# Performance work log

Measured on AMD Instinct MI355X. Metric: run time of the kernel, lower is better.

The kernel has to match this reference:

```python
import jax, jax.numpy as jnp
import numpy as np

D_MODEL = 2048
N_HEADS = 16
D_HEAD = 128
D_LATENT = 512


def setup_inputs() -> dict:
    key = jax.random.key(0)
    ks = jax.random.split(key, 5)
    s = lambda fan_in: 1.0 / np.sqrt(fan_in)
    x = jax.random.normal(ks[0], (2, 2048, D_MODEL), dtype=jnp.float32)
    # nn.Linear weights stored as [out, in]; we keep [in, out] for x @ W
    W_q = jax.random.uniform(ks[1], (D_MODEL, N_HEADS * D_HEAD), jnp.float32, -s(D_MODEL), s(D_MODEL))
    W_kv_down = jax.random.uniform(ks[2], (D_MODEL, D_LATENT), jnp.float32, -s(D_MODEL), s(D_MODEL))
    W_kv_up = jax.random.uniform(ks[3], (D_LATENT, N_HEADS * D_HEAD), jnp.float32, -s(D_LATENT), s(D_LATENT))
    W_o = jax.random.uniform(ks[4], (N_HEADS * D_HEAD, D_MODEL), jnp.float32, -s(N_HEADS * D_HEAD), s(N_HEADS * D_HEAD))
    return {"x": x, "W_q": W_q, "W_kv_down": W_kv_down, "W_kv_up": W_kv_up, "W_o": W_o}


def reference(x, W_q, W_kv_down, W_kv_up, W_o):
    B, S, _ = x.shape
    # q: [B, H, S, Dh]
    q = (x @ W_q).reshape(B, S, N_HEADS, D_HEAD).transpose(0, 2, 1, 3)
    # latent compression then up-projection; shared K = V
    latent = x @ W_kv_down                      # [B, S, Dl]
    kv = (latent @ W_kv_up).reshape(B, S, N_HEADS, D_HEAD).transpose(0, 2, 1, 3)
    scale = 1.0 / np.sqrt(D_HEAD).astype(np.float32)
    scores = jnp.einsum('bhqd,bhkd->bhqk', q, kv) * scale  # [B,H,S,S]
    probs = jax.nn.softmax(scores, axis=-1)
    out = jnp.einsum('bhqk,bhkd->bhqd', probs, kv)          # [B,H,S,Dh]
    out = out.transpose(0, 2, 1, 3).reshape(B, S, N_HEADS * D_HEAD)
    return out @ W_o
```

## Files before the change

### kernel.cpp

```cpp
#include <hip/hip_runtime.h>

typedef __attribute__((ext_vector_type(8))) __bf16 bf16x8;
typedef __attribute__((ext_vector_type(4))) float f32x4;
typedef __attribute__((ext_vector_type(16))) float f32x16;
typedef __attribute__((ext_vector_type(8))) unsigned short u16x8;
typedef __attribute__((ext_vector_type(4))) unsigned short u16x4;
typedef __attribute__((ext_vector_type(2))) unsigned int u32x2;
typedef __attribute__((ext_vector_type(4))) unsigned int u32x4;

#define MFMA16(a, b, c) __builtin_amdgcn_mfma_f32_16x16x32_bf16((a), (b), (c), 0, 0, 0)
#define MFMA32(a, b, c) __builtin_amdgcn_mfma_f32_32x32x16_bf16((a), (b), (c), 0, 0, 0)

__device__ __forceinline__ unsigned short f2bf(float f) {
    unsigned int u = __float_as_uint(f);
    unsigned int r = (u + 0x7FFFu + ((u >> 16) & 1u)) >> 16;
    return (unsigned short)r;
}

__device__ __forceinline__ float fexp2(float x) {
#if __has_builtin(__builtin_amdgcn_exp2f)
    return __builtin_amdgcn_exp2f(x);
#else
    return exp2f(x);
#endif
}

__device__ __forceinline__ u32x2 plswap32(unsigned int x, unsigned int y) {
#if __has_builtin(__builtin_amdgcn_permlane32_swap)
    return __builtin_amdgcn_permlane32_swap(x, y, false, false);
#else
    asm volatile("s_nop 1\n\tv_permlane32_swap_b32 %0, %1" : "+v"(x), "+v"(y));
    u32x2 r = {x, y};
    return r;
#endif
}
__device__ __forceinline__ u32x2 plswap16(unsigned int x, unsigned int y) {
#if __has_builtin(__builtin_amdgcn_permlane16_swap)
    return __builtin_amdgcn_permlane16_swap(x, y, false, false);
#else
    asm volatile("s_nop 1\n\tv_permlane16_swap_b32 %0, %1" : "+v"(x), "+v"(y));
    u32x2 r = {x, y};
    return r;
#endif
}

__device__ __forceinline__ float quad_reduce(float v) {
    u32x2 a = plswap32(__float_as_uint(v), __float_as_uint(v));
    v = __uint_as_float(a.x) + __uint_as_float(a.y);
    u32x2 b = plswap16(__float_as_uint(v), __float_as_uint(v));
    return __uint_as_float(b.x) + __uint_as_float(b.y);
}

__device__ __forceinline__ void transpose_tile(const float* __restrict__ in,
                                               unsigned short* __restrict__ out,
                                               int R, int C, int bx, int by) {
    __shared__ float tile[32][33];
    const int tx = threadIdx.x & 31, ty = threadIdx.x >> 5;
    const int c0 = bx * 32, r0 = by * 32;
#pragma unroll
    for (int i = 0; i < 4; ++i)
        tile[ty + i * 8][tx] = in[(size_t)(r0 + ty + i * 8) * C + c0 + tx];
    __syncthreads();
#pragma unroll
    for (int i = 0; i < 4; ++i)
        out[(size_t)(c0 + ty + i * 8) * R + r0 + tx] = f2bf(tile[tx][ty + i * 8]);
}

__global__ __launch_bounds__(256) void k_prep(const float* __restrict__ x,
                                              const float* __restrict__ Wq,
                                              const float* __restrict__ Wkvd,
                                              const float* __restrict__ Wkvu,
                                              const float* __restrict__ Wo,
                                              unsigned short* __restrict__ xb,
                                              unsigned short* __restrict__ Wcat_t,
                                              unsigned short* __restrict__ Wkvu_t,
                                              unsigned short* __restrict__ Wo_t) {
    const int i = blockIdx.x;
    if (i < 8192) {
        const int idx = i * 256 + threadIdx.x;
        const float4 v = ((const float4*)x)[idx];
        u16x4 o = { f2bf(v.x), f2bf(v.y), f2bf(v.z), f2bf(v.w) };
        ((u16x4*)xb)[idx] = o;
    } else if (i < 12288) {
        const int j = i - 8192;
        transpose_tile(Wq, Wcat_t, 2048, 2048, j & 63, j >> 6);
    } else if (i < 13312) {
        const int j = i - 12288;
        transpose_tile(Wkvd, Wcat_t + 2048 * 2048, 2048, 512, j & 15, j >> 4);
    } else if (i < 14336) {
        const int j = i - 13312;
        transpose_tile(Wkvu, Wkvu_t, 512, 2048, j & 63, j >> 6);
    } else {
        const int j = i - 14336;
        transpose_tile(Wo, Wo_t, 2048, 2048, j & 63, j >> 6);
    }
}

template <int OUT_MODE>
__global__ __launch_bounds__(256) void k_gemm_bt(const unsigned short* __restrict__ A,
                                                 const unsigned short* __restrict__ B,
                                                 void* __restrict__ Cv,
                                                 unsigned short* __restrict__ Ct,
                                                 int M, int N, int K, float alpha) {
    __shared__ alignas(16) unsigned short As[2 * 128 * 32];
    __shared__ alignas(16) unsigned short Bs[2 * 128 * 32];
    const int tid = threadIdx.x;
    const int wave = tid >> 6;
    const int lane = tid & 63;
    const int l16 = lane & 15;
    const int quad = lane >> 4;
    const int bm = blockIdx.x * 128;
    const int bn = blockIdx.y * 128;
    const int wm = (wave >> 1) * 64;
    const int wn = (wave & 1) * 64;

    const f32x4 fzero = {0.f, 0.f, 0.f, 0.f};
    f32x4 acc[4][4];
#pragma unroll
    for (int i = 0; i < 4; ++i)
#pragma unroll
        for (int j = 0; j < 4; ++j) acc[i][j] = fzero;

    auto AsL = (__attribute__((address_space(3))) unsigned short*)As;
    auto BsL = (__attribute__((address_space(3))) unsigned short*)Bs;

    const int c0 = wave * 128 + lane;

    auto stage = [&](int kt32) {
        const int boff = (kt32 & 1) * (128 * 32);
        const int kt = kt32 * 32;
#pragma unroll
        for (int j = 0; j < 2; ++j) {
            const int c = c0 + j * 64;
            __builtin_amdgcn_global_load_lds(
                (const __attribute__((address_space(1))) void*)(A + (size_t)(bm + (c >> 2)) * K + kt + (c & 3) * 8),
                (__attribute__((address_space(3))) void*)(AsL + boff + c * 8), 16, 0, 0);
            __builtin_amdgcn_global_load_lds(
                (const __attribute__((address_space(1))) void*)(B + (size_t)(bn + (c >> 2)) * K + kt + (c & 3) * 8),
                (__attribute__((address_space(3))) void*)(BsL + boff + c * 8), 16, 0, 0);
        }
    };

    const int nk = K >> 5;
    stage(0);
    for (int kt32 = 0; kt32 < nk; ++kt32) {
        __syncthreads();
        if (kt32 + 1 < nk) stage(kt32 + 1);
        const unsigned short* Ab = As + (kt32 & 1) * (128 * 32);
        const unsigned short* Bb = Bs + (kt32 & 1) * (128 * 32);

        bf16x8 af[4], bfr[4];
#pragma unroll
        for (int mt = 0; mt < 4; ++mt)
            af[mt] = *(const bf16x8*)(Ab + (wm + mt * 16 + l16) * 32 + quad * 8);
#pragma unroll
        for (int nt = 0; nt < 4; ++nt)
            bfr[nt] = *(const bf16x8*)(Bb + (wn + nt * 16 + l16) * 32 + quad * 8);
#pragma unroll
        for (int mt = 0; mt < 4; ++mt)
#pragma unroll
            for (int nt = 0; nt < 4; ++nt)
                acc[mt][nt] = MFMA16(af[mt], bfr[nt], acc[mt][nt]);
    }

#pragma unroll
    for (int mt = 0; mt < 4; ++mt)
#pragma unroll
        for (int nt = 0; nt < 4; ++nt) {
            const int row0 = bm + wm + mt * 16 + quad * 4;
            const int col = bn + wn + nt * 16 + l16;
            u16x4 pk;
#pragma unroll
            for (int r = 0; r < 4; ++r) {
                const float v0 = acc[mt][nt][r];
                if (OUT_MODE == 0) {
                    ((float*)Cv)[(size_t)(row0 + r) * N + col] = v0 * alpha;
                } else if (OUT_MODE == 3) {
                    if (col < 2048)
                        ((unsigned short*)Cv)[(size_t)(row0 + r) * 2048 + col] = f2bf(v0 * alpha);
                    else
                        Ct[(size_t)(row0 + r) * 512 + (col - 2048)] = f2bf(v0);
                } else {
                    const unsigned short b = f2bf(v0 * alpha);
                    ((unsigned short*)Cv)[(size_t)(row0 + r) * N + col] = b;
                    pk[r] = b;
                }
            }
            if (OUT_MODE == 2) {
                const size_t ti =
                    ((size_t)((row0 >> 11) * (N >> 7) + (col >> 7)) * 128 + (col & 127)) * 2048 +
                    (row0 & 2047);
                *(u16x4*)(Ct + ti) = pk;
            }
        }
}

__global__ __launch_bounds__(256, 2) void k_attn(const unsigned short* __restrict__ Q,
                                                 const unsigned short* __restrict__ KV,
                                                 const unsigned short* __restrict__ KVT,
                                                 unsigned short* __restrict__ O) {
    __shared__ alignas(16) unsigned short Ks[2 * 64 * 128];
    __shared__ alignas(16) unsigned short Vt[2 * 128 * 64];

    const int tid = threadIdx.x;
    const int wave = tid >> 6, lane = tid & 63;
    const int q31 = lane & 31;
    const int hi = lane >> 5;
    const int l8 = q31 & 7;
    const int lid = blockIdx.x + (blockIdx.y << 4);
    const int wid = ((lid & 7) << 6) + (lid >> 3);
    const int qt = wid & 15;
    const int bh = wid >> 4;
    const size_t tokbase = (size_t)(bh >> 4) * 2048;
    const int hcol = (bh & 15) * 128;
    const unsigned short* kvt_head = KVT + (size_t)bh * (128 * 2048);

    bf16x8 qf[8];
    const int qrow0 = qt * 128 + wave * 32;
    {
        const unsigned short* qp = Q + (tokbase + qrow0 + q31) * 2048 + hcol + hi * 8;
#pragma unroll
        for (int kd = 0; kd < 8; ++kd) qf[kd] = *(const bf16x8*)(qp + kd * 16);
    }

    f32x16 o_acc[4];
#pragma unroll
    for (int dt = 0; dt < 4; ++dt)
#pragma unroll
        for (int r = 0; r < 16; ++r) o_acc[dt][r] = 0.f;
    float l_i = 0.f;

    auto KsL = (__attribute__((address_space(3))) unsigned short*)Ks;
    auto VtL = (__attribute__((address_space(3))) unsigned short*)Vt;

    const int r4 = tid >> 4, cdK = tid & 15;
    const int csK = (cdK & 8) | ((cdK & 7) ^ (r4 & 7));
    const int dv = tid >> 3, cvV = tid & 7;
    const int csV = cvV ^ (dv & 7);
    const unsigned short* kp0 = KV + (tokbase + r4) * 2048 + hcol + csK * 8;
    const unsigned short* vp0 = kvt_head + (size_t)dv * 2048 + csV * 8;

    auto stage = [&](int kt) {
        auto Kb = KsL + (kt & 1) * (64 * 128) + tid * 8;
        auto Vb = VtL + (kt & 1) * (128 * 64) + tid * 8;
        const unsigned short* kp = kp0 + (size_t)kt * (64 * 2048);
        const unsigned short* vp = vp0 + kt * 64;
#pragma unroll
        for (int p = 0; p < 4; ++p) {
            __builtin_amdgcn_global_load_lds(
                (const __attribute__((address_space(1))) void*)(kp + p * (16 * 2048)),
                (__attribute__((address_space(3))) void*)(Kb + p * 2048), 16, 0, 0);
            __builtin_amdgcn_global_load_lds(
                (const __attribute__((address_space(1))) void*)(vp + (size_t)p * (32 * 2048)),
                (__attribute__((address_space(3))) void*)(Vb + p * 2048), 16, 0, 0);
        }
    };

    stage(0);

    for (int kt = 0; kt < 32; ++kt) {
        __syncthreads();
        if (kt < 31) stage(kt + 1);
        const unsigned short* Kb = Ks + (kt & 1) * (64 * 128);
        const unsigned short* Vb = Vt + (kt & 1) * (128 * 64);

        f32x16 st[2];
#pragma unroll
        for (int r = 0; r < 16; ++r) { st[0][r] = 0.f; st[1][r] = 0.f; }
        __builtin_amdgcn_s_setprio(1);
#pragma unroll
        for (int kd = 0; kd < 8; ++kd) {
            const int c = 2 * kd + hi;
            const int sw = (c & 8) | ((c & 7) ^ l8);
#pragma unroll
            for (int mt = 0; mt < 2; ++mt) {
                const bf16x8 kf = *(const bf16x8*)(Kb + (mt * 32 + q31) * 128 + sw * 8);
                st[mt] = MFMA32(kf, qf[kd], st[mt]);
            }
        }
        __builtin_amdgcn_s_setprio(0);

        bf16x8 pfrk[2][2];
#pragma unroll
        for (int mt = 0; mt < 2; ++mt) {
            float p[16];
            float rs = 0.f;
#pragma unroll
            for (int r = 0; r < 16; ++r) {
                p[r] = fexp2(st[mt][r]);
                rs += p[r];
            }
            l_i += rs;
#pragma unroll
            for (int s = 0; s < 2; ++s) {
                unsigned int w0, w1, w2, w3;
                asm("v_cvt_pk_bf16_f32 %0, %1, %2" : "=v"(w0) : "v"(p[s * 8 + 0]), "v"(p[s * 8 + 1]));
                asm("v_cvt_pk_bf16_f32 %0, %1, %2" : "=v"(w1) : "v"(p[s * 8 + 2]), "v"(p[s * 8 + 3]));
                asm("v_cvt_pk_bf16_f32 %0, %1, %2" : "=v"(w2) : "v"(p[s * 8 + 4]), "v"(p[s * 8 + 5]));
                asm("v_cvt_pk_bf16_f32 %0, %1, %2" : "=v"(w3) : "v"(p[s * 8 + 6]), "v"(p[s * 8 + 7]));
                const u32x2 u02 = plswap32(w0, w2);
                const u32x2 u13 = plswap32(w1, w3);
                const u32x4 w = {u02.x, u13.x, u02.y, u13.y};
                pfrk[mt][s] = __builtin_bit_cast(bf16x8, w);
            }
        }

        __builtin_amdgcn_s_setprio(1);
#pragma unroll
        for (int ks = 0; ks < 4; ++ks) {
            const int swv = ((2 * ks + hi) ^ l8) * 8;
            const bf16x8 pf = pfrk[ks >> 1][ks & 1];
#pragma unroll
            for (int dt = 0; dt < 4; ++dt) {
                const bf16x8 vf = *(const bf16x8*)(Vb + (dt * 32 + q31) * 64 + swv);
                o_acc[dt] = MFMA32(vf, pf, o_acc[dt]);
            }
        }
        __builtin_amdgcn_s_setprio(0);
    }

    {
        const u32x2 a = plswap32(__float_as_uint(l_i), __float_as_uint(l_i));
        const float inv = 1.0f / (__uint_as_float(a.x) + __uint_as_float(a.y));
        unsigned short* dst = O + (tokbase + qrow0 + q31) * 2048 + hcol + hi * 4;
#pragma unroll
        for (int dt = 0; dt < 4; ++dt)
#pragma unroll
            for (int g = 0; g < 4; ++g) {
                u16x4 pk;
#pragma unroll
                for (int j = 0; j < 4; ++j) pk[j] = f2bf(o_acc[dt][g * 4 + j] * inv);
                *(u16x4*)(dst + dt * 32 + g * 8) = pk;
            }
    }
}

extern "C" void kernel_launch(void* const* d_in, const int* in_sizes, int n_in,
                              void* d_out, int out_size, void* d_ws, size_t ws_size,
                              hipStream_t stream) {
    const float* x = (const float*)d_in[0];
    const float* W_q = (const float*)d_in[1];
    const float* W_kvd = (const float*)d_in[2];
    const float* W_kvu = (const float*)d_in[3];
    const float* W_o = (const float*)d_in[4];

    char* w = (char*)d_ws;
    unsigned short* xb = (unsigned short*)(w);
    unsigned short* kvT = xb;
    unsigned short* qb = (unsigned short*)(w + (size_t)16 * 1024 * 1024);
    unsigned short* kvb = (unsigned short*)(w + (size_t)32 * 1024 * 1024);
    unsigned short* Wo_t = (unsigned short*)(w + (size_t)48 * 1024 * 1024);
    unsigned short* Wcat_t = (unsigned short*)(w + (size_t)56 * 1024 * 1024);
    unsigned short* Wkvu_t = (unsigned short*)(w + (size_t)66 * 1024 * 1024);
    unsigned short* lat = (unsigned short*)(w + (size_t)68 * 1024 * 1024);

    k_prep<<<18432, 256, 0, stream>>>(x, W_q, W_kvd, W_kvu, W_o, xb, Wcat_t, Wkvu_t, Wo_t);

    k_gemm_bt<3><<<dim3(32, 20), 256, 0, stream>>>(xb, Wcat_t, qb, lat, 4096, 2560, 2048,
                                                   0.12751743f);
    k_gemm_bt<2><<<dim3(32, 16), 256, 0, stream>>>(lat, Wkvu_t, kvb, kvT, 4096, 2048, 512,
                                                   1.0f);
    k_attn<<<dim3(16, 32), 256, 0, stream>>>(qb, kvb, kvT, qb);
    k_gemm_bt<0><<<dim3(32, 16), 256, 0, stream>>>(qb, Wo_t, d_out, nullptr, 4096, 2048, 2048,
                                                   1.0f);
}
```

Measured before the change: 309.9 us.

## Add 256x256-tile triple-buffered GEMM with direct global-to-LDS loads for projections

```diff
diff --git a/kernel.cpp b/kernel.cpp
--- a/kernel.cpp
+++ b/kernel.cpp
@@ -10,6 +10,7 @@
 
 #define MFMA16(a, b, c) __builtin_amdgcn_mfma_f32_16x16x32_bf16((a), (b), (c), 0, 0, 0)
 #define MFMA32(a, b, c) __builtin_amdgcn_mfma_f32_32x32x16_bf16((a), (b), (c), 0, 0, 0)
+#define WAITVM(n) asm volatile("s_waitcnt vmcnt(" #n ")" ::: "memory")
 
 __device__ __forceinline__ unsigned short f2bf(float f) {
     unsigned int u = __float_as_uint(f);
@@ -33,22 +34,6 @@
     u32x2 r = {x, y};
     return r;
 #endif
-}
-__device__ __forceinline__ u32x2 plswap16(unsigned int x, unsigned int y) {
-#if __has_builtin(__builtin_amdgcn_permlane16_swap)
-    return __builtin_amdgcn_permlane16_swap(x, y, false, false);
-#else
-    asm volatile("s_nop 1\n\tv_permlane16_swap_b32 %0, %1" : "+v"(x), "+v"(y));
-    u32x2 r = {x, y};
-    return r;
-#endif
-}
-
-__device__ __forceinline__ float quad_reduce(float v) {
-    u32x2 a = plswap32(__float_as_uint(v), __float_as_uint(v));
-    v = __uint_as_float(a.x) + __uint_as_float(a.y);
-    u32x2 b = plswap16(__float_as_uint(v), __float_as_uint(v));
-    return __uint_as_float(b.x) + __uint_as_float(b.y);
 }
 
 __device__ __forceinline__ void transpose_tile(const float* __restrict__ in,
@@ -173,24 +158,118 @@
 #pragma unroll
             for (int r = 0; r < 4; ++r) {
                 const float v0 = acc[mt][nt][r];
-                if (OUT_MODE == 0) {
-                    ((float*)Cv)[(size_t)(row0 + r) * N + col] = v0 * alpha;
-                } else if (OUT_MODE == 3) {
-                    if (col < 2048)
-                        ((unsigned short*)Cv)[(size_t)(row0 + r) * 2048 + col] = f2bf(v0 * alpha);
-                    else
-                        Ct[(size_t)(row0 + r) * 512 + (col - 2048)] = f2bf(v0);
-                } else {
-                    const unsigned short b = f2bf(v0 * alpha);
-                    ((unsigned short*)Cv)[(size_t)(row0 + r) * N + col] = b;
-                    pk[r] = b;
-                }
+                const unsigned short b = f2bf(v0 * alpha);
+                ((unsigned short*)Cv)[(size_t)(row0 + r) * N + col] = b;
+                pk[r] = b;
             }
             if (OUT_MODE == 2) {
                 const size_t ti =
                     ((size_t)((row0 >> 11) * (N >> 7) + (col >> 7)) * 128 + (col & 127)) * 2048 +
                     (row0 & 2047);
                 *(u16x4*)(Ct + ti) = pk;
+            }
+        }
+}
+
+template <int OUT_MODE>
+__global__ __launch_bounds__(512, 2) void k_gemm256(const unsigned short* __restrict__ A,
+                                                    const unsigned short* __restrict__ B,
+                                                    void* __restrict__ Cv,
+                                                    unsigned short* __restrict__ Ct,
+                                                    int M, int N, int K, float alpha) {
+    extern __shared__ unsigned short sm[];
+    unsigned short* As = sm;
+    unsigned short* Bs = sm + 3 * 256 * 32;
+    const int tid = threadIdx.x;
+    const int wave = tid >> 6;
+    const int lane = tid & 63;
+    const int l16 = lane & 15;
+    const int quad = lane >> 4;
+    const int bm = blockIdx.x * 256;
+    const int bn = blockIdx.y * 256;
+    const int wm = (wave >> 2) * 128;
+    const int wn = (wave & 3) * 64;
+
+    const f32x4 fzero = {0.f, 0.f, 0.f, 0.f};
+    f32x4 acc[8][4];
+#pragma unroll
+    for (int i = 0; i < 8; ++i)
+#pragma unroll
+        for (int j = 0; j < 4; ++j) acc[i][j] = fzero;
+
+    auto AsL = (__attribute__((address_space(3))) unsigned short*)As;
+    auto BsL = (__attribute__((address_space(3))) unsigned short*)Bs;
+
+    const int rstage = tid >> 2;
+    const int cs = (tid & 3) ^ (((tid >> 5) & 1) << 1) ^ ((tid >> 3) & 1);
+    const unsigned short* ap0 = A + (size_t)(bm + rstage) * K + cs * 8;
+    const unsigned short* bp0 = B + (size_t)(bn + rstage) * K + cs * 8;
+
+    auto stage = [&](int kt) {
+        const int buf = kt % 3;
+        auto Ad = AsL + buf * 8192 + tid * 8;
+        auto Bd = BsL + buf * 8192 + tid * 8;
+        const unsigned short* ap = ap0 + kt * 32;
+        const unsigned short* bp = bp0 + kt * 32;
+#pragma unroll
+        for (int p = 0; p < 2; ++p) {
+            __builtin_amdgcn_global_load_lds(
+                (const __attribute__((address_space(1))) void*)(ap + (size_t)p * 128 * K),
+                (__attribute__((address_space(3))) void*)(Ad + p * 4096), 16, 0, 0);
+            __builtin_amdgcn_global_load_lds(
+                (const __attribute__((address_space(1))) void*)(bp + (size_t)p * 128 * K),
+                (__attribute__((address_space(3))) void*)(Bd + p * 4096), 16, 0, 0);
+        }
+    };
+
+    const int cq = quad ^ (((l16 >> 3) & 1) << 1) ^ ((l16 >> 1) & 1);
+
+    const int nk = K >> 5;
+    stage(0);
+    stage(1);
+
+    for (int kt = 0; kt < nk; ++kt) {
+        if (kt + 1 < nk) { WAITVM(4); } else { WAITVM(0); }
+        __builtin_amdgcn_s_barrier();
+        if (kt + 2 < nk) stage(kt + 2);
+
+        const unsigned short* Ab = As + (kt % 3) * 8192;
+        const unsigned short* Bb = Bs + (kt % 3) * 8192;
+
+        bf16x8 af[8], bfr[4];
+#pragma unroll
+        for (int mf = 0; mf < 8; ++mf)
+            af[mf] = *(const bf16x8*)(Ab + (wm + mf * 16 + l16) * 32 + cq * 8);
+#pragma unroll
+        for (int nf = 0; nf < 4; ++nf)
+            bfr[nf] = *(const bf16x8*)(Bb + (wn + nf * 16 + l16) * 32 + cq * 8);
+
+        __builtin_amdgcn_s_setprio(1);
+#pragma unroll
+        for (int mf = 0; mf < 8; ++mf)
+#pragma unroll
+            for (int nf = 0; nf < 4; ++nf)
+                acc[mf][nf] = MFMA16(af[mf], bfr[nf], acc[mf][nf]);
+        __builtin_amdgcn_s_setprio(0);
+    }
+
+#pragma unroll
+    for (int mf = 0; mf < 8; ++mf)
+#pragma unroll
+        for (int nf = 0; nf < 4; ++nf) {
+            const int row0 = bm + wm + mf * 16 + quad * 4;
+            const int col = bn + wn + nf * 16 + l16;
+#pragma unroll
+            for (int r = 0; r < 4; ++r) {
+                const float v0 = acc[mf][nf][r];
+                if (OUT_MODE == 0) {
+                    ((float*)Cv)[(size_t)(row0 + r) * N + col] = v0 * alpha;
+                } else {
+                    if (col < 2048)
+                        ((unsigned short*)Cv)[(size_t)(row0 + r) * 2048 + col] = f2bf(v0 * alpha);
+                    else
+                        Ct[(size_t)(row0 + r) * 512 + (col - 2048)] = f2bf(v0);
+                }
             }
         }
 }
@@ -354,13 +433,22 @@
     unsigned short* Wkvu_t = (unsigned short*)(w + (size_t)66 * 1024 * 1024);
     unsigned short* lat = (unsigned short*)(w + (size_t)68 * 1024 * 1024);
 
+    static bool attr_done = false;
+    if (!attr_done) {
+        hipFuncSetAttribute(reinterpret_cast<const void*>(k_gemm256<3>),
+                            hipFuncAttributeMaxDynamicSharedMemorySize, 98304);
+        hipFuncSetAttribute(reinterpret_cast<const void*>(k_gemm256<0>),
+                            hipFuncAttributeMaxDynamicSharedMemorySize, 98304);
+        attr_done = true;
+    }
+
     k_prep<<<18432, 256, 0, stream>>>(x, W_q, W_kvd, W_kvu, W_o, xb, Wcat_t, Wkvu_t, Wo_t);
 
-    k_gemm_bt<3><<<dim3(32, 20), 256, 0, stream>>>(xb, Wcat_t, qb, lat, 4096, 2560, 2048,
-                                                   0.12751743f);
+    k_gemm256<3><<<dim3(16, 10), 512, 98304, stream>>>(xb, Wcat_t, qb, lat, 4096, 2560,
+                                                       2048, 0.12751743f);
     k_gemm_bt<2><<<dim3(32, 16), 256, 0, stream>>>(lat, Wkvu_t, kvb, kvT, 4096, 2048, 512,
                                                    1.0f);
     k_attn<<<dim3(16, 32), 256, 0, stream>>>(qb, kvb, kvT, qb);
-    k_gemm_bt<0><<<dim3(32, 16), 256, 0, stream>>>(qb, Wo_t, d_out, nullptr, 4096, 2048, 2048,
-                                                   1.0f);
-}
+    k_gemm256<0><<<dim3(16, 8), 512, 98304, stream>>>(qb, Wo_t, d_out, nullptr, 4096, 2048,
+                                                      2048, 1.0f);
+}
```

Result: slower. 323.5 us (+4.4%).
